# Kernel optimization log

Measured on AMD Instinct MI355X. Metric: run time of the kernel, lower is better.

Reference implementation:

```python
import jax, jax.numpy as jnp
import numpy as np


def deform_conv2d(x, w, offset, mask, pad):
    """Modulated deformable conv (DCNv2), stride 1, dilation 1, groups 1.
    x: [B,C,H,W], w: [Co,C,kh,kw], offset: [B,2*K,H,W] (y,x per tap), mask: [B,K,H,W].
    Output spatial size equals input (pad = (k-1)//2).
    """
    B, C, H, W = x.shape
    Co, _, kh, kw = w.shape
    K = kh * kw
    off = offset.reshape(B, K, 2, H, W)
    dy, dx = off[:, :, 0], off[:, :, 1]               # [B,K,H,W]
    ky, kx = jnp.meshgrid(jnp.arange(kh), jnp.arange(kw), indexing='ij')
    ky = ky.reshape(K).astype(x.dtype)
    kx = kx.reshape(K).astype(x.dtype)
    hh = jnp.arange(H, dtype=x.dtype)
    ww = jnp.arange(W, dtype=x.dtype)
    # sampling coords: p0 + p_k + delta p_k
    py = hh[None, None, :, None] - pad + ky[None, :, None, None] + dy  # [B,K,H,W]
    px = ww[None, None, None, :] - pad + kx[None, :, None, None] + dx
    y0 = jnp.floor(py)
    x0 = jnp.floor(px)
    wy = py - y0
    wx = px - x0
    y0i = y0.astype(jnp.int32)
    x0i = x0.astype(jnp.int32)
    x_flat = x.reshape(B, C, H * W)

    def gather(yi, xi):
        valid = (yi >= 0) & (yi < H) & (xi >= 0) & (xi < W)  # zero padding outside
        idx = jnp.clip(yi, 0, H - 1) * W + jnp.clip(xi, 0, W - 1)
        g = jnp.take_along_axis(x_flat, idx.reshape(B, 1, K * H * W), axis=2)
        g = g.reshape(B, C, K, H, W)
        return g * valid[:, None].astype(x.dtype)

    v00 = gather(y0i, x0i)
    v01 = gather(y0i, x0i + 1)
    v10 = gather(y0i + 1, x0i)
    v11 = gather(y0i + 1, x0i + 1)
    wy_ = wy[:, None]  # [B,1,K,H,W]
    wx_ = wx[:, None]
    samp = (v00 * (1 - wy_) * (1 - wx_) + v01 * (1 - wy_) * wx_
            + v10 * wy_ * (1 - wx_) + v11 * wy_ * wx_)   # [B,C,K,H,W]
    # masked weighted accumulation == conv over sampled taps
    return jnp.einsum('bckhw,bkhw,ock->bohw', samp, mask, w.reshape(Co, C, K))


def setup_inputs() -> dict:
    key = jax.random.key(0)
    ks = jax.random.split(key, 10)
    B, C, H, W, Co = 4, 64, 64, 64, 64
    inp = {
        'x': jax.random.normal(ks[0], (B, C, H, W), dtype=jnp.float32),
        'filter1': jax.random.normal(ks[1], (Co, C, 3, 3), dtype=jnp.float32) * 0.05,
        'offset1': jax.random.normal(ks[2], (B, 2 * 9, H, W), dtype=jnp.float32),
        'mask1': jax.random.uniform(ks[3], (B, 9, H, W), dtype=jnp.float32),
        'filter2': jax.random.normal(ks[4], (Co, C, 5, 5), dtype=jnp.float32) * 0.03,
        'offset2': jax.random.normal(ks[5], (B, 2 * 25, H, W), dtype=jnp.float32),
        'mask2': jax.random.uniform(ks[6], (B, 25, H, W), dtype=jnp.float32),
        'filter3': jax.random.normal(ks[7], (Co, C, 7, 7), dtype=jnp.float32) * 0.02,
        'offset3': jax.random.normal(ks[8], (B, 2 * 49, H, W), dtype=jnp.float32),
        'mask3': jax.random.uniform(ks[9], (B, 49, H, W), dtype=jnp.float32),
    }
    return inp


def reference(x, filter1, offset1, mask1, filter2, offset2, mask2, filter3, offset3, mask3):
    part1 = deform_conv2d(x, filter1, offset1, mask1, pad=1)  # 3x3
    part2 = deform_conv2d(x, filter2, offset2, mask2, pad=2)  # 5x5
    part3 = deform_conv2d(x, filter3, offset3, mask3, pad=3)  # 7x7
    return jnp.concatenate((part1, part2, part3), axis=1)
```

## Files before the change

kernel.cpp:

```cpp
#include <hip/hip_runtime.h>
#include <hip/hip_bf16.h>


typedef __attribute__((ext_vector_type(8))) short bf16x8;
typedef __attribute__((ext_vector_type(8))) unsigned short u16x8;
typedef __attribute__((ext_vector_type(4))) float f32x4;
typedef __attribute__((ext_vector_type(2))) float f32x2;

#define WR 16
#define WC 30
#define WS 68
#define SLS 20

__device__ __forceinline__ unsigned short f2bf(float f) {
    __hip_bfloat16 h = __float2bfloat16(f);
    return *reinterpret_cast<unsigned short*>(&h);
}
__device__ __forceinline__ f32x2 unpk(unsigned u) {
    f32x2 r;
    r[0] = __uint_as_float(u << 16);
    r[1] = __uint_as_float(u & 0xffff0000u);
    return r;
}

__global__ __launch_bounds__(256) void k_prep(
    const float* __restrict__ x,
    const float* __restrict__ f1, const float* __restrict__ f2, const float* __restrict__ f3,
    unsigned short* __restrict__ xTb,
    unsigned short* __restrict__ wp1, unsigned short* __restrict__ wp2, unsigned short* __restrict__ wp3) {
    __shared__ float tile[64][65];
    int bid = blockIdx.x;
    int tid = threadIdx.x;
    if (bid < 256) {
        int b = bid >> 6, h = bid & 63;
        {
            int w = tid & 63, c4 = tid >> 6;
            const float* xp = x + (((b * 64) * 64 + h) * 64) + w;
            #pragma unroll
            for (int i = 0; i < 16; ++i) {
                int c = c4 * 16 + i;
                tile[c][w] = xp[c * 4096];
            }
        }
        __syncthreads();
        {
            int c = tid & 63, w4 = tid >> 6;
            unsigned short* op = xTb + (((b * 64 + h) * 64) * 64) + c;
            #pragma unroll
            for (int i = 0; i < 16; ++i) {
                int ww = w4 * 16 + i;
                op[ww * 64] = f2bf(tile[c][ww]);
            }
        }
    } else {
        int idx = (bid - 256) * 256 + tid;
        const float* f; unsigned short* wp; int K, rel;
        if (idx < 36864)       { f = f1; wp = wp1; K = 9;  rel = idx; }
        else if (idx < 139264) { f = f2; wp = wp2; K = 25; rel = idx - 36864; }
        else                   { f = f3; wp = wp3; K = 49; rel = idx - 139264; }
        int k    = rel >> 12;
        int r2   = rel & 4095;
        int ct   = r2 >> 10;
        int cg   = (r2 >> 9) & 1;
        int lane = (r2 >> 3) & 63;
        int j    = r2 & 7;
        int o = ct * 16 + (lane & 15);
        int c = cg * 32 + (lane >> 4) * 8 + j;
        wp[rel] = f2bf(f[(o * 64 + c) * K + k]);
    }
}

template<int KW, int PAD, int KS, int KE>
__device__ __forceinline__ void run_range(
    const float* __restrict__ offp, const float* __restrict__ mskp,
    const unsigned short* __restrict__ wpF, const unsigned short* __restrict__ win,
    const unsigned short* __restrict__ xb,
    int h, int pw, int ylo, int cxlo, int ch0, int lofs, f32x4 acc[4]) {

    constexpr int NT = KE - KS;

    float dys[NT], dxs[NT], mks[NT];
    #pragma unroll
    for (int i = 0; i < NT; ++i) {
        dys[i] = offp[(KS + i) * 8192];
        dxs[i] = offp[(KS + i) * 8192 + 4096];
        mks[i] = mskp[(KS + i) * 4096];
    }

    #pragma unroll
    for (int i = 0; i < NT; ++i) {
        const int k = KS + i;
        const int ky = k / KW, kx = k - ky * KW;
        float dy = dys[i];
        float dx = dxs[i];
        float mk = mks[i];
        float py = (float)(h - PAD + ky) + dy;
        float px = (float)(pw - PAD + kx) + dx;
        float y0f = floorf(py), x0f = floorf(px);
        float wy = py - y0f, wx = px - x0f;
        int y0 = (int)y0f, x0 = (int)x0f;
        int y1 = y0 + 1, x1 = x0 + 1;
        float fy0 = ((unsigned)y0 < 64u) ? (1.f - wy) * mk : 0.f;
        float fy1 = ((unsigned)y1 < 64u) ? wy * mk         : 0.f;
        float gx0 = ((unsigned)x0 < 64u) ? (1.f - wx)      : 0.f;
        float gx1 = ((unsigned)x1 < 64u) ? wx              : 0.f;
        float w00 = fy0 * gx0, w01 = fy0 * gx1, w10 = fy1 * gx0, w11 = fy1 * gx1;

        int r0 = y0 - ylo, r1 = r0 + 1;
        int c0 = x0 - cxlo, c1 = c0 + 1;
        bool oow = ((w00 != 0.f) & (((unsigned)r0 >= WR) | ((unsigned)c0 >= WC)))
                 | ((w01 != 0.f) & (((unsigned)r0 >= WR) | ((unsigned)c1 >= WC)))
                 | ((w10 != 0.f) & (((unsigned)r1 >= WR) | ((unsigned)c0 >= WC)))
                 | ((w11 != 0.f) & (((unsigned)r1 >= WR) | ((unsigned)c1 >= WC)));
        int r0c = min(max(r0, 0), WR - 1), r1c = min(max(r1, 0), WR - 1);
        int c0c = min(max(c0, 0), WC - 1), c1c = min(max(c1, 0), WC - 1);
        int p00 = (r0c * WC + c0c) * WS;
        int p01 = (r0c * WC + c1c) * WS;
        int p10 = (r1c * WC + c0c) * WS;
        int p11 = (r1c * WC + c1c) * WS;

        union U { u16x8 v; unsigned u[4]; };
        U g00a, g01a, g10a, g11a, g00b, g01b, g10b, g11b;
        g00a.v = *(const u16x8*)(win + p00 + ch0);
        g01a.v = *(const u16x8*)(win + p01 + ch0);
        g10a.v = *(const u16x8*)(win + p10 + ch0);
        g11a.v = *(const u16x8*)(win + p11 + ch0);
        g00b.v = *(const u16x8*)(win + p00 + 32 + ch0);
        g01b.v = *(const u16x8*)(win + p01 + 32 + ch0);
        g10b.v = *(const u16x8*)(win + p10 + 32 + ch0);
        g11b.v = *(const u16x8*)(win + p11 + 32 + ch0);

        if (oow) {
            int y0g = min(max(y0, 0), 63), y1g = min(max(y1, 0), 63);
            int x0g = min(max(x0, 0), 63), x1g = min(max(x1, 0), 63);
            int o00 = ((y0g << 6) + x0g) << 6;
            int o01 = ((y0g << 6) + x1g) << 6;
            int o10 = ((y1g << 6) + x0g) << 6;
            int o11 = ((y1g << 6) + x1g) << 6;
            g00a.v = *(const u16x8*)(xb + o00 + ch0);
            g01a.v = *(const u16x8*)(xb + o01 + ch0);
            g10a.v = *(const u16x8*)(xb + o10 + ch0);
            g11a.v = *(const u16x8*)(xb + o11 + ch0);
            g00b.v = *(const u16x8*)(xb + o00 + 32 + ch0);
            g01b.v = *(const u16x8*)(xb + o01 + 32 + ch0);
            g10b.v = *(const u16x8*)(xb + o10 + 32 + ch0);
            g11b.v = *(const u16x8*)(xb + o11 + 32 + ch0);
        }

        f32x2 W00 = {w00, w00}, W01 = {w01, w01}, W10 = {w10, w10}, W11 = {w11, w11};
        union { bf16x8 v; unsigned short u[8]; } A0, A1;
        #pragma unroll
        for (int j2 = 0; j2 < 4; ++j2) {
            f32x2 s0 = W00 * unpk(g00a.u[j2]) + W01 * unpk(g01a.u[j2])
                     + W10 * unpk(g10a.u[j2]) + W11 * unpk(g11a.u[j2]);
            f32x2 s1 = W00 * unpk(g00b.u[j2]) + W01 * unpk(g01b.u[j2])
                     + W10 * unpk(g10b.u[j2]) + W11 * unpk(g11b.u[j2]);
            A0.u[2 * j2]     = f2bf(s0[0]);
            A0.u[2 * j2 + 1] = f2bf(s0[1]);
            A1.u[2 * j2]     = f2bf(s1[0]);
            A1.u[2 * j2 + 1] = f2bf(s1[1]);
        }

        const unsigned short* wpk = wpF + (k << 12) + lofs;
        #pragma unroll
        for (int ct = 0; ct < 4; ++ct) {
            bf16x8 b0 = *(const bf16x8*)(wpk + ct * 1024);
            bf16x8 b1 = *(const bf16x8*)(wpk + ct * 1024 + 512);
            acc[ct] = __builtin_amdgcn_mfma_f32_16x16x32_bf16(A0.v, b0, acc[ct], 0, 0, 0);
            acc[ct] = __builtin_amdgcn_mfma_f32_16x16x32_bf16(A1.v, b1, acc[ct], 0, 0, 0);
        }
    }
}

__global__ __launch_bounds__(512, 4) void k_dcn(
    const unsigned short* __restrict__ xTb,
    const float* __restrict__ off1, const float* __restrict__ msk1, const unsigned short* __restrict__ wp1,
    const float* __restrict__ off2, const float* __restrict__ msk2, const unsigned short* __restrict__ wp2,
    const float* __restrict__ off3, const float* __restrict__ msk3, const unsigned short* __restrict__ wp3,
    float* __restrict__ out) {

    __shared__ __align__(16) unsigned char smem[WR * WC * WS * 2];
    unsigned short* win = (unsigned short*)smem;
    float* slab = (float*)smem;

    int tile = blockIdx.x;
    int b  = tile >> 8;
    int h  = (tile >> 2) & 63;
    int w0 = (tile & 3) << 4;

    int tid  = threadIdx.x;
    int wv   = tid >> 6;
    int lane = tid & 63;
    int quad = lane >> 4;
    int l16  = lane & 15;
    int ylo  = h - 7, cxlo = w0 - 7;

    const unsigned short* xb = xTb + ((size_t)b << 18);

    {
        int j = tid & 7;
        for (int p = tid >> 3; p < WR * WC; p += 64) {
            int r = p / WC, cc = p - r * WC;
            int y = min(max(ylo + r, 0), 63);
            int x = min(max(cxlo + cc, 0), 63);
            *(u16x8*)(win + p * WS + j * 8) =
                *(const u16x8*)(xb + (((y << 6) + x) << 6) + j * 8);
        }
    }
    __syncthreads();

    int pw   = w0 + l16;
    int ch0  = quad << 3;
    int lofs = lane << 3;
    const float* o1p = off1 + (b * 18) * 4096 + (h << 6) + pw;
    const float* m1p = msk1 + (b * 9)  * 4096 + (h << 6) + pw;
    const float* o2p = off2 + (b * 50) * 4096 + (h << 6) + pw;
    const float* m2p = msk2 + (b * 25) * 4096 + (h << 6) + pw;
    const float* o3p = off3 + (b * 98) * 4096 + (h << 6) + pw;
    const float* m3p = msk3 + (b * 49) * 4096 + (h << 6) + pw;

    f32x4 accA[4], accB[4];
    #pragma unroll
    for (int i = 0; i < 4; ++i) { accA[i] = (f32x4){0,0,0,0}; accB[i] = (f32x4){0,0,0,0}; }
    int slabA, slabB = -1;

    switch (wv) {
        case 0:
            run_range<3,1,0,9>  (o1p, m1p, wp1, win, xb, h, pw, ylo, cxlo, ch0, lofs, accA);
            slabA = 0; break;
        case 1:
            run_range<5,2,0,11> (o2p, m2p, wp2, win, xb, h, pw, ylo, cxlo, ch0, lofs, accA);
            slabA = 1; break;
        case 2:
            run_range<5,2,11,22>(o2p, m2p, wp2, win, xb, h, pw, ylo, cxlo, ch0, lofs, accA);
            slabA = 2; break;
        case 3:
            run_range<5,2,22,25>(o2p, m2p, wp2, win, xb, h, pw, ylo, cxlo, ch0, lofs, accA);
            slabA = 3;
            run_range<7,3,0,8>  (o3p, m3p, wp3, win, xb, h, pw, ylo, cxlo, ch0, lofs, accB);
            slabB = 4; break;
        case 4:
            run_range<7,3,8,18> (o3p, m3p, wp3, win, xb, h, pw, ylo, cxlo, ch0, lofs, accA);
            slabA = 5; break;
        case 5:
            run_range<7,3,18,28>(o3p, m3p, wp3, win, xb, h, pw, ylo, cxlo, ch0, lofs, accA);
            slabA = 6; break;
        case 6:
            run_range<7,3,28,38>(o3p, m3p, wp3, win, xb, h, pw, ylo, cxlo, ch0, lofs, accA);
            slabA = 7; break;
        default:
            run_range<7,3,38,49>(o3p, m3p, wp3, win, xb, h, pw, ylo, cxlo, ch0, lofs, accA);
            slabA = 8; break;
    }

    __syncthreads();

    #pragma unroll
    for (int ct = 0; ct < 4; ++ct) {
        *(f32x4*)&slab[slabA * 1280 + (ct * 16 + l16) * SLS + quad * 4] = accA[ct];
    }
    if (slabB >= 0) {
        #pragma unroll
        for (int ct = 0; ct < 4; ++ct) {
            *(f32x4*)&slab[slabB * 1280 + (ct * 16 + l16) * SLS + quad * 4] = accB[ct];
        }
    }
    __syncthreads();

    for (int it = tid; it < 768; it += 512) {
        int g = it & 3;
        int o = it >> 2;
        int oo = o & 63;
        int base = oo * SLS + g * 4;
        f32x4 v;
        if (o < 64) {
            v = *(const f32x4*)&slab[base];
        } else if (o < 128) {
            f32x4 a0 = *(const f32x4*)&slab[1 * 1280 + base];
            f32x4 a1 = *(const f32x4*)&slab[2 * 1280 + base];
            f32x4 a2 = *(const f32x4*)&slab[3 * 1280 + base];
            #pragma unroll
            for (int r = 0; r < 4; ++r) v[r] = a0[r] + (a1[r] + a2[r]);
        } else {
            f32x4 a0 = *(const f32x4*)&slab[4 * 1280 + base];
            f32x4 a1 = *(const f32x4*)&slab[5 * 1280 + base];
            f32x4 a2 = *(const f32x4*)&slab[6 * 1280 + base];
            f32x4 a3 = *(const f32x4*)&slab[7 * 1280 + base];
            f32x4 a4 = *(const f32x4*)&slab[8 * 1280 + base];
            #pragma unroll
            for (int r = 0; r < 4; ++r) v[r] = (a0[r] + a1[r]) + (a2[r] + a3[r]) + a4[r];
        }
        *(f32x4*)&out[(((size_t)b * 192 + o) * 64 + h) * 64 + w0 + g * 4] = v;
    }
}

extern "C" void kernel_launch(void* const* d_in, const int* in_sizes, int n_in,
                              void* d_out, int out_size, void* d_ws, size_t ws_size,
                              hipStream_t stream) {
    const float* x    = (const float*)d_in[0];
    const float* f1   = (const float*)d_in[1];
    const float* off1 = (const float*)d_in[2];
    const float* msk1 = (const float*)d_in[3];
    const float* f2   = (const float*)d_in[4];
    const float* off2 = (const float*)d_in[5];
    const float* msk2 = (const float*)d_in[6];
    const float* f3   = (const float*)d_in[7];
    const float* off3 = (const float*)d_in[8];
    const float* msk3 = (const float*)d_in[9];
    float* out = (float*)d_out;

    unsigned short* xTb = (unsigned short*)d_ws;
    unsigned short* wp1 = xTb + 4 * 64 * 64 * 64;
    unsigned short* wp2 = wp1 + 9 * 4096;
    unsigned short* wp3 = wp2 + 25 * 4096;

    k_prep<<<dim3(1584), dim3(256), 0, stream>>>(x, f1, f2, f3, xTb, wp1, wp2, wp3);
    k_dcn<<<dim3(1024), dim3(512), 0, stream>>>(xTb,
                                                off1, msk1, wp1,
                                                off2, msk2, wp2,
                                                off3, msk3, wp3,
                                                out);
}
```

Before: 169.3 us.

## Replace templated unrolled tap ranges with runtime loop and rebalance wave split

Replaces the per-wave templated, fully unrolled tap ranges with a single runtime loop whose tap range is chosen by a switch on the wave index. Each wave now owns exactly one accumulator slab, and the taps are redistributed (12/13 for 5x5, about 10 per wave for 7x7) so the wave that did double duty disappears and the load is flatter. Offset and mask values are prefetched one tap ahead in software instead of being loaded all up front, which cuts register pressure and code size. In exchange, tap indices are no longer compile-time constants and the loop is no longer unrolled, which can reduce instruction-level parallelism.

```diff
diff --git a/kernel.cpp b/kernel.cpp
--- a/kernel.cpp
+++ b/kernel.cpp
@@ -70,40 +70,89 @@
     }
 }
 
-template<int KW, int PAD, int KS, int KE>
-__device__ __forceinline__ void run_range(
-    const float* __restrict__ offp, const float* __restrict__ mskp,
-    const unsigned short* __restrict__ wpF, const unsigned short* __restrict__ win,
-    const unsigned short* __restrict__ xb,
-    int h, int pw, int ylo, int cxlo, int ch0, int lofs, f32x4 acc[4]) {
-
-    constexpr int NT = KE - KS;
-
-    float dys[NT], dxs[NT], mks[NT];
+__global__ __launch_bounds__(512, 4) void k_dcn(
+    const unsigned short* __restrict__ xTb,
+    const float* __restrict__ off1, const float* __restrict__ msk1, const unsigned short* __restrict__ wp1,
+    const float* __restrict__ off2, const float* __restrict__ msk2, const unsigned short* __restrict__ wp2,
+    const float* __restrict__ off3, const float* __restrict__ msk3, const unsigned short* __restrict__ wp3,
+    float* __restrict__ out) {
+
+    __shared__ __align__(16) unsigned char smem[WR * WC * WS * 2];
+    unsigned short* win = (unsigned short*)smem;
+    float* slab = (float*)smem;
+
+    int tile = blockIdx.x;
+    int b  = tile >> 8;
+    int h  = (tile >> 2) & 63;
+    int w0 = (tile & 3) << 4;
+
+    int tid  = threadIdx.x;
+    int wv   = tid >> 6;
+    int lane = tid & 63;
+    int quad = lane >> 4;
+    int l16  = lane & 15;
+    int ylo  = h - 7, cxlo = w0 - 7;
+
+    const unsigned short* xb = xTb + ((size_t)b << 18);
+
+    {
+        int j = tid & 7;
+        for (int p = tid >> 3; p < WR * WC; p += 64) {
+            int r = p / WC, cc = p - r * WC;
+            int y = min(max(ylo + r, 0), 63);
+            int x = min(max(cxlo + cc, 0), 63);
+            *(u16x8*)(win + p * WS + j * 8) =
+                *(const u16x8*)(xb + (((y << 6) + x) << 6) + j * 8);
+        }
+    }
+    __syncthreads();
+
+    int pw   = w0 + l16;
+    int ch0  = quad << 3;
+    int lofs = lane << 3;
+
+    const float* offs; const float* msks; const unsigned short* wpF;
+    int ks, ke, kw, pad;
+    switch (wv) {
+        case 0:  offs = off1; msks = msk1; wpF = wp1; kw = 3; pad = 1; ks = 0;  ke = 9;  break;
+        case 1:  offs = off2; msks = msk2; wpF = wp2; kw = 5; pad = 2; ks = 0;  ke = 12; break;
+        case 2:  offs = off2; msks = msk2; wpF = wp2; kw = 5; pad = 2; ks = 12; ke = 25; break;
+        case 3:  offs = off3; msks = msk3; wpF = wp3; kw = 7; pad = 3; ks = 0;  ke = 10; break;
+        case 4:  offs = off3; msks = msk3; wpF = wp3; kw = 7; pad = 3; ks = 10; ke = 20; break;
+        case 5:  offs = off3; msks = msk3; wpF = wp3; kw = 7; pad = 3; ks = 20; ke = 30; break;
+        case 6:  offs = off3; msks = msk3; wpF = wp3; kw = 7; pad = 3; ks = 30; ke = 40; break;
+        default: offs = off3; msks = msk3; wpF = wp3; kw = 7; pad = 3; ks = 40; ke = 49; break;
+    }
+    int K2 = (kw == 3) ? 9 : (kw == 5) ? 25 : 49;
+    const float* offp = offs + ((b * 2 * K2) * 4096) + (h << 6) + pw;
+    const float* mskp = msks + ((b * K2) * 4096) + (h << 6) + pw;
+
+    f32x4 acc[4];
     #pragma unroll
-    for (int i = 0; i < NT; ++i) {
-        dys[i] = offp[(KS + i) * 8192];
-        dxs[i] = offp[(KS + i) * 8192 + 4096];
-        mks[i] = mskp[(KS + i) * 4096];
-    }
-
-    #pragma unroll
-    for (int i = 0; i < NT; ++i) {
-        const int k = KS + i;
-        const int ky = k / KW, kx = k - ky * KW;
-        float dy = dys[i];
-        float dx = dxs[i];
-        float mk = mks[i];
-        float py = (float)(h - PAD + ky) + dy;
-        float px = (float)(pw - PAD + kx) + dx;
+    for (int i = 0; i < 4; ++i) acc[i] = (f32x4){0.f, 0.f, 0.f, 0.f};
+
+    int ky = ks / kw, kx = ks - ky * kw;
+
+    float dyC = offp[ks * 8192];
+    float dxC = offp[ks * 8192 + 4096];
+    float mkC = mskp[ks * 4096];
+
+    for (int k = ks; k < ke; ++k) {
+        int kn = min(k + 1, ke - 1);
+        float dyN = offp[kn * 8192];
+        float dxN = offp[kn * 8192 + 4096];
+        float mkN = mskp[kn * 4096];
+
+        float py = (float)(h - pad + ky) + dyC;
+        float px = (float)(pw - pad + kx) + dxC;
         float y0f = floorf(py), x0f = floorf(px);
         float wy = py - y0f, wx = px - x0f;
         int y0 = (int)y0f, x0 = (int)x0f;
         int y1 = y0 + 1, x1 = x0 + 1;
-        float fy0 = ((unsigned)y0 < 64u) ? (1.f - wy) * mk : 0.f;
-        float fy1 = ((unsigned)y1 < 64u) ? wy * mk         : 0.f;
-        float gx0 = ((unsigned)x0 < 64u) ? (1.f - wx)      : 0.f;
-        float gx1 = ((unsigned)x1 < 64u) ? wx              : 0.f;
+        float fy0 = ((unsigned)y0 < 64u) ? (1.f - wy) * mkC : 0.f;
+        float fy1 = ((unsigned)y1 < 64u) ? wy * mkC         : 0.f;
+        float gx0 = ((unsigned)x0 < 64u) ? (1.f - wx)       : 0.f;
+        float gx1 = ((unsigned)x1 < 64u) ? wx               : 0.f;
         float w00 = fy0 * gx0, w01 = fy0 * gx1, w10 = fy1 * gx0, w11 = fy1 * gx1;
 
         int r0 = y0 - ylo, r1 = r0 + 1;
@@ -169,101 +218,16 @@
             acc[ct] = __builtin_amdgcn_mfma_f32_16x16x32_bf16(A0.v, b0, acc[ct], 0, 0, 0);
             acc[ct] = __builtin_amdgcn_mfma_f32_16x16x32_bf16(A1.v, b1, acc[ct], 0, 0, 0);
         }
-    }
-}
-
-__global__ __launch_bounds__(512, 4) void k_dcn(
-    const unsigned short* __restrict__ xTb,
-    const float* __restrict__ off1, const float* __restrict__ msk1, const unsigned short* __restrict__ wp1,
-    const float* __restrict__ off2, const float* __restrict__ msk2, const unsigned short* __restrict__ wp2,
-    const float* __restrict__ off3, const float* __restrict__ msk3, const unsigned short* __restrict__ wp3,
-    float* __restrict__ out) {
-
-    __shared__ __align__(16) unsigned char smem[WR * WC * WS * 2];
-    unsigned short* win = (unsigned short*)smem;
-    float* slab = (float*)smem;
-
-    int tile = blockIdx.x;
-    int b  = tile >> 8;
-    int h  = (tile >> 2) & 63;
-    int w0 = (tile & 3) << 4;
-
-    int tid  = threadIdx.x;
-    int wv   = tid >> 6;
-    int lane = tid & 63;
-    int quad = lane >> 4;
-    int l16  = lane & 15;
-    int ylo  = h - 7, cxlo = w0 - 7;
-
-    const unsigned short* xb = xTb + ((size_t)b << 18);
-
-    {
-        int j = tid & 7;
-        for (int p = tid >> 3; p < WR * WC; p += 64) {
-            int r = p / WC, cc = p - r * WC;
-            int y = min(max(ylo + r, 0), 63);
-            int x = min(max(cxlo + cc, 0), 63);
-            *(u16x8*)(win + p * WS + j * 8) =
-                *(const u16x8*)(xb + (((y << 6) + x) << 6) + j * 8);
-        }
-    }
-    __syncthreads();
-
-    int pw   = w0 + l16;
-    int ch0  = quad << 3;
-    int lofs = lane << 3;
-    const float* o1p = off1 + (b * 18) * 4096 + (h << 6) + pw;
-    const float* m1p = msk1 + (b * 9)  * 4096 + (h << 6) + pw;
-    const float* o2p = off2 + (b * 50) * 4096 + (h << 6) + pw;
-    const float* m2p = msk2 + (b * 25) * 4096 + (h << 6) + pw;
-    const float* o3p = off3 + (b * 98) * 4096 + (h << 6) + pw;
-    const float* m3p = msk3 + (b * 49) * 4096 + (h << 6) + pw;
-
-    f32x4 accA[4], accB[4];
-    #pragma unroll
-    for (int i = 0; i < 4; ++i) { accA[i] = (f32x4){0,0,0,0}; accB[i] = (f32x4){0,0,0,0}; }
-    int slabA, slabB = -1;
-
-    switch (wv) {
-        case 0:
-            run_range<3,1,0,9>  (o1p, m1p, wp1, win, xb, h, pw, ylo, cxlo, ch0, lofs, accA);
-            slabA = 0; break;
-        case 1:
-            run_range<5,2,0,11> (o2p, m2p, wp2, win, xb, h, pw, ylo, cxlo, ch0, lofs, accA);
-            slabA = 1; break;
-        case 2:
-            run_range<5,2,11,22>(o2p, m2p, wp2, win, xb, h, pw, ylo, cxlo, ch0, lofs, accA);
-            slabA = 2; break;
-        case 3:
-            run_range<5,2,22,25>(o2p, m2p, wp2, win, xb, h, pw, ylo, cxlo, ch0, lofs, accA);
-            slabA = 3;
-            run_range<7,3,0,8>  (o3p, m3p, wp3, win, xb, h, pw, ylo, cxlo, ch0, lofs, accB);
-            slabB = 4; break;
-        case 4:
-            run_range<7,3,8,18> (o3p, m3p, wp3, win, xb, h, pw, ylo, cxlo, ch0, lofs, accA);
-            slabA = 5; break;
-        case 5:
-            run_range<7,3,18,28>(o3p, m3p, wp3, win, xb, h, pw, ylo, cxlo, ch0, lofs, accA);
-            slabA = 6; break;
-        case 6:
-            run_range<7,3,28,38>(o3p, m3p, wp3, win, xb, h, pw, ylo, cxlo, ch0, lofs, accA);
-            slabA = 7; break;
-        default:
-            run_range<7,3,38,49>(o3p, m3p, wp3, win, xb, h, pw, ylo, cxlo, ch0, lofs, accA);
-            slabA = 8; break;
+
+        dyC = dyN; dxC = dxN; mkC = mkN;
+        if (++kx == kw) { kx = 0; ++ky; }
     }
 
     __syncthreads();
 
     #pragma unroll
     for (int ct = 0; ct < 4; ++ct) {
-        *(f32x4*)&slab[slabA * 1280 + (ct * 16 + l16) * SLS + quad * 4] = accA[ct];
-    }
-    if (slabB >= 0) {
-        #pragma unroll
-        for (int ct = 0; ct < 4; ++ct) {
-            *(f32x4*)&slab[slabB * 1280 + (ct * 16 + l16) * SLS + quad * 4] = accB[ct];
-        }
+        *(f32x4*)&slab[wv * 1280 + (ct * 16 + l16) * SLS + quad * 4] = acc[ct];
     }
     __syncthreads();
 
@@ -278,15 +242,14 @@
         } else if (o < 128) {
             f32x4 a0 = *(const f32x4*)&slab[1 * 1280 + base];
             f32x4 a1 = *(const f32x4*)&slab[2 * 1280 + base];
-            f32x4 a2 = *(const f32x4*)&slab[3 * 1280 + base];
-            #pragma unroll
-            for (int r = 0; r < 4; ++r) v[r] = a0[r] + (a1[r] + a2[r]);
+            #pragma unroll
+            for (int r = 0; r < 4; ++r) v[r] = a0[r] + a1[r];
         } else {
-            f32x4 a0 = *(const f32x4*)&slab[4 * 1280 + base];
-            f32x4 a1 = *(const f32x4*)&slab[5 * 1280 + base];
-            f32x4 a2 = *(const f32x4*)&slab[6 * 1280 + base];
-            f32x4 a3 = *(const f32x4*)&slab[7 * 1280 + base];
-            f32x4 a4 = *(const f32x4*)&slab[8 * 1280 + base];
+            f32x4 a0 = *(const f32x4*)&slab[3 * 1280 + base];
+            f32x4 a1 = *(const f32x4*)&slab[4 * 1280 + base];
+            f32x4 a2 = *(const f32x4*)&slab[5 * 1280 + base];
+            f32x4 a3 = *(const f32x4*)&slab[6 * 1280 + base];
+            f32x4 a4 = *(const f32x4*)&slab[7 * 1280 + base];
             #pragma unroll
             for (int r = 0; r < 4; ++r) v[r] = (a0[r] + a1[r]) + (a2[r] + a3[r]) + a4[r];
         }
```

Result: faster. 165.4 us (-2.3%).
